# Kernel tuning notes

Hardware: AMD Instinct MI355X
Metric: run time of the kernel (lower is better)

## Reference

```python
import jax, jax.numpy as jnp
import numpy as np

N_GT, N_NODES, N_SPECIES, N_EDGES, D, L = 512, 399, 200, 397, 64, 2


def setup_inputs() -> dict:
    rng = np.random.default_rng(0)
    # Random recursive trees: parent of node i is uniform in [0, i).
    par = (rng.random((N_GT, N_NODES - 1)) * np.arange(1, N_NODES)).astype(np.int64)
    child = np.broadcast_to(np.arange(1, N_NODES), (N_GT, N_NODES - 1))
    off = (np.arange(N_GT, dtype=np.int64) * N_NODES)[:, None]
    c = (child + off).ravel()
    p = (par + off).ravel()
    # Both directions, as in the original [2, 2E_gt] convention.
    edge_index = np.stack([np.concatenate([c, p]), np.concatenate([p, c])])
    sp = np.full(N_NODES, -1, dtype=np.int64)
    sp[:N_SPECIES] = np.arange(N_SPECIES)
    sp_ids = np.tile(sp, N_GT)
    leaf_mask = sp_ids >= 0
    batch_vec = np.repeat(np.arange(N_GT, dtype=np.int64), N_NODES)
    # Clades: random species subsets per species-tree edge, guaranteed nonempty.
    pe = rng.uniform(0.05, 0.5, (N_EDGES, 1))
    clade_mask = rng.random((N_EDGES, N_SPECIES)) < pe
    clade_mask[np.arange(N_EDGES), rng.integers(0, N_SPECIES, N_EDGES)] = True
    key = jax.random.key(0)
    ks = jax.random.split(key, 3)
    s = 1.0 / np.sqrt(D)
    return {
        "edge_index": jnp.asarray(edge_index),
        "sp_ids": jnp.asarray(sp_ids),
        "leaf_mask": jnp.asarray(leaf_mask),
        "batch_vec": jnp.asarray(batch_vec),
        "clade_mask": jnp.asarray(clade_mask),
        "n_gt": N_GT,
        "emb_table": jax.random.normal(ks[0], (N_SPECIES + 1, D), jnp.float32),
        "W1": jax.random.normal(ks[1], (L, D, D), jnp.float32) * s,
        "b1": jnp.zeros((L, D), jnp.float32),
        "W2": jax.random.normal(ks[2], (L, D, D), jnp.float32) * s,
        "b2": jnp.zeros((L, D), jnp.float32),
        "eps": jnp.zeros((L,), jnp.float32),  # GINConv train_eps init 0
        "ln_gamma": jnp.ones((L, D), jnp.float32),
        "ln_beta": jnp.zeros((L, D), jnp.float32),
    }


def _layernorm(x, g, b):
    mu = x.mean(-1, keepdims=True)
    var = ((x - mu) ** 2).mean(-1, keepdims=True)
    return (x - mu) * jax.lax.rsqrt(var + 1e-5) * g + b


def reference(edge_index, sp_ids, leaf_mask, batch_vec, clade_mask, n_gt,
              emb_table, W1, b1, W2, b2, eps, ln_gamma, ln_beta):
    n_nodes = sp_ids.shape[0]
    n_edges, n_species = clade_mask.shape
    d = emb_table.shape[1]
    # Species embedding (internal nodes -> extra row n_species).
    emb_ids = jnp.where(sp_ids < 0, n_species, sp_ids)
    x = emb_table[emb_ids]  # [Nn, D]
    src, dst = edge_index[0], edge_index[1]
    for l in range(W1.shape[0]):
        # GINConv: mlp((1+eps)*x + sum_neighbors x_j), residual, LayerNorm.
        msg = jax.ops.segment_sum(x[src], dst, num_segments=n_nodes)
        h = (1.0 + eps[l]) * x + msg
        h = jax.nn.relu(h @ W1[l] + b1[l]) @ W2[l] + b2[l]
        x = _layernorm(x + h, ln_gamma[l], ln_beta[l])
        # dropout is identity in eval mode
    # Species pooling: mean over valid leaves per (gene tree, species).
    w = (leaf_mask & (sp_ids >= 0)).astype(x.dtype)  # [Nn]
    comp = batch_vec * n_species + jnp.maximum(sp_ids, 0)
    pool_size = n_gt * n_species
    sums = jax.ops.segment_sum(x * w[:, None], comp, num_segments=pool_size)
    cnts = jax.ops.segment_sum(w, comp, num_segments=pool_size)
    pool = (sums / jnp.maximum(cnts, 1.0)[:, None]).reshape(n_gt, n_species, d)
    valid = (cnts > 0).astype(x.dtype).reshape(n_gt, n_species)  # [G, S]
    # Clade pooling per species-tree edge (vectorized over the per-edge loop).
    mf = clade_mask.astype(x.dtype)  # [E, S]
    csum = jnp.einsum('es,gsd->egd', mf, pool * valid[:, :, None])  # [E,G,D]
    ccnt = mf @ valid.T  # [E, G] valid-species count per (edge, gene tree)
    gt_means = csum / jnp.maximum(ccnt, 1.0)[:, :, None]
    has = (ccnt > 0).astype(x.dtype)  # gene trees with data for this edge
    n_v = has.sum(1)  # [E]
    mean = (gt_means * has[:, :, None]).sum(1) / jnp.maximum(n_v, 1.0)[:, None]
    diff = (gt_means - mean[:, None, :]) * has[:, :, None]
    var = (diff ** 2).sum(1) / jnp.maximum(n_v - 1.0, 1.0)[:, None]  # unbiased
    ok = (n_v > 1)[:, None]
    std = jnp.where(ok, jnp.sqrt(jnp.where(ok, var, 1.0)), 0.0)
    mean = jnp.where((n_v > 0)[:, None], mean, 0.0)
    return jnp.concatenate([mean, std], axis=-1)  # [n_edges, 2*D]
```

## Files before the change

### kernel.cpp

```cpp
#include <hip/hip_runtime.h>

#define SMAX 200
#define NPG 399

typedef __bf16 bf16x8 __attribute__((ext_vector_type(8)));
typedef _Float16 half8 __attribute__((ext_vector_type(8)));
typedef float f32x4 __attribute__((ext_vector_type(4)));

__device__ __forceinline__ unsigned short f2bf(float f) {
  unsigned u = __float_as_uint(f);
  unsigned r = (u + 0x7FFFu + ((u >> 16) & 1u)) >> 16;
  return (unsigned short)r;
}
__device__ __forceinline__ int xel(int node, int dim) {
  return node * 64 + ((((dim >> 3)) ^ (node & 7)) << 3) + (dim & 7);
}

__global__ __launch_bounds__(256) void k_prep(const int* __restrict__ clade,
                                              unsigned short* __restrict__ mfA,
                                              unsigned* __restrict__ mfbits,
                                              int n_edges, int n_species) {
  int stride = gridDim.x * 256;
  for (int idx = blockIdx.x * 256 + threadIdx.x; idx < 25 * 7 * 512;
       idx += stride) {
    int fi = idx >> 9, within = idx & 511;
    int mt = fi / 7, kt = fi % 7;
    int l = within >> 3, j = within & 7;
    int e = mt * 16 + (l & 15);
    int s = kt * 32 + ((l >> 4) & 3) * 8 + j;
    unsigned short v = 0;
    if (e < n_edges && s < n_species && clade[(size_t)e * n_species + s] != 0)
      v = 0x3F80;
    mfA[idx] = v;
  }
  for (int idx = blockIdx.x * 256 + threadIdx.x; idx < 400 * 8; idx += stride) {
    int e = idx >> 3, w = idx & 7;
    unsigned bits = 0;
    if (e < n_edges && w < 7) {
      for (int b = 0; b < 32; ++b) {
        int s = w * 32 + b;
        if (s < n_species && clade[(size_t)e * n_species + s] != 0)
          bits |= 1u << b;
      }
    }
    mfbits[idx] = bits;
  }
}

__global__ __launch_bounds__(512) void k_tree(
    const float* __restrict__ emb, const int* __restrict__ sp,
    const int* __restrict__ leaf, const int* __restrict__ src,
    const int* __restrict__ dst, const float* __restrict__ W1,
    const float* __restrict__ b1, const float* __restrict__ W2,
    const float* __restrict__ b2, const float* __restrict__ eps_p,
    const float* __restrict__ gam, const float* __restrict__ bet,
    const unsigned short* __restrict__ mfA, const unsigned* __restrict__ mfbits,
    _Float16* __restrict__ gmat, float* __restrict__ has, int npg,
    int n_species, int n_edges, int n_gt) {
  __shared__ __attribute__((aligned(16))) _Float16 sA[NPG * 64];
  __shared__ __attribute__((aligned(16))) _Float16 sB[NPG * 64];
  __shared__ __attribute__((aligned(16))) _Float16 sWf[2][2][4096];
  __shared__ __attribute__((aligned(16))) _Float16 sT[8][1024];
  __shared__ int sStart[NPG + 1];
  __shared__ int sChild[NPG - 1];
  __shared__ int sPar[NPG];
  __shared__ int sCnt[NPG];

  int g = blockIdx.x, tid = threadIdx.x;
  int base = g * npg, nEt = npg - 1, ebase = g * nEt;
  int w = tid >> 6, lane = tid & 63;
  int cc = lane & 15, gq = lane >> 4;

  for (int i = tid; i < npg + 1; i += 512) sStart[i] = 0;
  for (int i = tid; i < npg; i += 512) sCnt[i] = 0;
  __syncthreads();
  for (int idx = tid; idx < 4096; idx += 512) {
    int k = idx >> 6, n = idx & 63;
    int frag = (k >> 5) * 4 + (n >> 4);
    int ln = ((k >> 3) & 3) * 16 + (n & 15);
    int j = k & 7;
    int o = frag * 512 + ln * 8 + j;
    sWf[0][0][o] = (_Float16)W1[idx];
    sWf[0][1][o] = (_Float16)W2[idx];
    sWf[1][0][o] = (_Float16)W1[4096 + idx];
    sWf[1][1][o] = (_Float16)W2[4096 + idx];
  }
  for (int idx = tid; idx < npg * 8; idx += 512) {
    int node = idx >> 3, ch = idx & 7;
    int s = sp[base + node];
    int row = (s < 0) ? n_species : s;
    float4 v0 = reinterpret_cast<const float4*>(emb)[row * 16 + ch * 2];
    float4 v1 = reinterpret_cast<const float4*>(emb)[row * 16 + ch * 2 + 1];
    half8 h;
    h[0] = (_Float16)v0.x; h[1] = (_Float16)v0.y;
    h[2] = (_Float16)v0.z; h[3] = (_Float16)v0.w;
    h[4] = (_Float16)v1.x; h[5] = (_Float16)v1.y;
    h[6] = (_Float16)v1.z; h[7] = (_Float16)v1.w;
    *reinterpret_cast<half8*>(&sA[node * 64 + ((ch ^ (node & 7)) << 3)]) = h;
  }
  for (int i = tid; i < nEt; i += 512) {
    int c = src[ebase + i] - base;
    int p = dst[ebase + i] - base;
    sPar[c] = p;
    atomicAdd(&sStart[p + 1], 1);
  }
  __syncthreads();
  if (w == 0) {
    int run = 0;
    for (int chunk = 0; chunk * 64 < npg + 1; ++chunk) {
      int idx = chunk * 64 + lane;
      int v = (idx < npg + 1) ? sStart[idx] : 0;
      for (int off = 1; off < 64; off <<= 1) {
        int t2 = __shfl_up(v, off);
        if (lane >= off) v += t2;
      }
      v += run;
      if (idx < npg + 1) sStart[idx] = v;
      run = __shfl(v, 63);
    }
  }
  __syncthreads();
  for (int c = tid + 1; c < npg; c += 512) {
    int p = sPar[c];
    int pos = sStart[p] + atomicAdd(&sCnt[p], 1);
    sChild[pos] = c;
  }
  __syncthreads();

  _Float16* tb = sT[w];
  int t0w = w * 3;
  int t1w = (w == 7) ? 25 : t0w + 3;
  for (int l = 0; l < 2; ++l) {
    const _Float16* xin = l ? sB : sA;
    _Float16* xout = l ? sA : sB;
    const half8* xin8 = reinterpret_cast<const half8*>(xin);
    float e1 = 1.0f + eps_p[l];
    float b1v[4], b2v[4], gv[4], bv[4];
#pragma unroll
    for (int nt = 0; nt < 4; ++nt) {
      b1v[nt] = b1[l * 64 + cc + 16 * nt];
      b2v[nt] = b2[l * 64 + cc + 16 * nt];
      gv[nt] = gam[l * 64 + cc + 16 * nt];
      bv[nt] = bet[l * 64 + cc + 16 * nt];
    }
    const half8* B1 = reinterpret_cast<const half8*>(sWf[l][0]);
    const half8* B2 = reinterpret_cast<const half8*>(sWf[l][1]);
    for (int t = t0w; t < t1w; ++t) {
      int n0 = t * 16;
      int node = n0 + cc;
      bool vn = node < npg;
      int nd2 = vn ? node : 0;
      int j0v = vn ? sStart[nd2] : 0;
      int cnt = vn ? (sStart[nd2 + 1] - j0v) : 0;
      half8 s0 = xin8[nd2 * 8 + (gq ^ (nd2 & 7))];
      half8 s1 = xin8[nd2 * 8 + ((4 + gq) ^ (nd2 & 7))];
      bool hasp = vn && node > 0;
      int pr = hasp ? sPar[nd2] : 0;
      half8 p0 = xin8[pr * 8 + (gq ^ (pr & 7))];
      half8 p1 = xin8[pr * 8 + ((4 + gq) ^ (pr & 7))];
      float a0f[8], a1f[8];
#pragma unroll
      for (int d = 0; d < 8; ++d) {
        a0f[d] = e1 * (float)s0[d] + (hasp ? (float)p0[d] : 0.f);
        a1f[d] = e1 * (float)s1[d] + (hasp ? (float)p1[d] : 0.f);
      }
      int cmax = cnt;
#pragma unroll
      for (int off = 1; off < 64; off <<= 1)
        cmax = max(cmax, __shfl_xor(cmax, off));
      cmax = __builtin_amdgcn_readfirstlane(cmax);
      for (int k0 = 0; k0 < cmax; k0 += 4) {
        int ci[4];
#pragma unroll
        for (int jj = 0; jj < 4; ++jj) {
          int kk = k0 + jj;
          ci[jj] = sChild[(kk < cnt) ? (j0v + kk) : 0];
        }
        half8 v0[4], v1[4];
#pragma unroll
        for (int jj = 0; jj < 4; ++jj) {
          int c = ci[jj];
          v0[jj] = xin8[c * 8 + (gq ^ (c & 7))];
          v1[jj] = xin8[c * 8 + ((4 + gq) ^ (c & 7))];
        }
#pragma unroll
        for (int jj = 0; jj < 4; ++jj) {
          if (k0 + jj < cnt) {
#pragma unroll
            for (int d = 0; d < 8; ++d) {
              a0f[d] += (float)v0[jj][d];
              a1f[d] += (float)v1[jj][d];
            }
          }
        }
      }
      half8 a0, a1;
#pragma unroll
      for (int d = 0; d < 8; ++d) {
        a0[d] = (_Float16)a0f[d];
        a1[d] = (_Float16)a1f[d];
      }
      f32x4 tacc[4];
#pragma unroll
      for (int nt = 0; nt < 4; ++nt) tacc[nt] = (f32x4){0.f, 0.f, 0.f, 0.f};
#pragma unroll
      for (int nt = 0; nt < 4; ++nt) {
        tacc[nt] = __builtin_amdgcn_mfma_f32_16x16x32_f16(
            a0, B1[nt * 64 + lane], tacc[nt], 0, 0, 0);
        tacc[nt] = __builtin_amdgcn_mfma_f32_16x16x32_f16(
            a1, B1[(4 + nt) * 64 + lane], tacc[nt], 0, 0, 0);
      }
#pragma unroll
      for (int nt = 0; nt < 4; ++nt)
#pragma unroll
        for (int r = 0; r < 4; ++r) {
          int m = gq * 4 + r;
          tb[m * 64 + ((cc + 16 * nt) ^ ((m & 7) << 3))] =
              (_Float16)fmaxf(tacc[nt][r] + b1v[nt], 0.f);
        }
      int sw = (cc & 7) << 3;
      half8 c0 =
          *reinterpret_cast<const half8*>(&tb[cc * 64 + ((gq * 8) ^ sw)]);
      half8 c1 =
          *reinterpret_cast<const half8*>(&tb[cc * 64 + ((32 + gq * 8) ^ sw)]);
      f32x4 hacc[4];
#pragma unroll
      for (int nt = 0; nt < 4; ++nt) hacc[nt] = (f32x4){0.f, 0.f, 0.f, 0.f};
#pragma unroll
      for (int nt = 0; nt < 4; ++nt) {
        hacc[nt] = __builtin_amdgcn_mfma_f32_16x16x32_f16(
            c0, B2[nt * 64 + lane], hacc[nt], 0, 0, 0);
        hacc[nt] = __builtin_amdgcn_mfma_f32_16x16x32_f16(
            c1, B2[(4 + nt) * 64 + lane], hacc[nt], 0, 0, 0);
      }
      float y[4][4];
#pragma unroll
      for (int r = 0; r < 4; ++r) {
        int nd3 = n0 + gq * 4 + r;
        bool v3 = nd3 < npg;
        int nds = v3 ? nd3 : 0;
#pragma unroll
        for (int nt = 0; nt < 4; ++nt) {
          float xv = (float)xin[xel(nds, cc + 16 * nt)];
          y[r][nt] = (v3 ? xv : 0.f) + hacc[nt][r] + b2v[nt];
        }
      }
#pragma unroll
      for (int r = 0; r < 4; ++r) {
        float s = y[r][0] + y[r][1] + y[r][2] + y[r][3];
        s += __shfl_xor(s, 1);
        s += __shfl_xor(s, 2);
        s += __shfl_xor(s, 4);
        s += __shfl_xor(s, 8);
        float mu = s * (1.f / 64.f);
        float d0 = y[r][0] - mu, d1 = y[r][1] - mu;
        float d2 = y[r][2] - mu, d3 = y[r][3] - mu;
        float v = d0 * d0 + d1 * d1 + d2 * d2 + d3 * d3;
        v += __shfl_xor(v, 1);
        v += __shfl_xor(v, 2);
        v += __shfl_xor(v, 4);
        v += __shfl_xor(v, 8);
        float iv = rsqrtf(v * (1.f / 64.f) + 1e-5f);
        int nd3 = n0 + gq * 4 + r;
        if (nd3 < npg) {
#pragma unroll
          for (int nt = 0; nt < 4; ++nt)
            xout[xel(nd3, cc + 16 * nt)] =
                (_Float16)((y[r][nt] - mu) * iv * gv[nt] + bv[nt]);
        }
      }
    }
    __syncthreads();
  }

  unsigned short* sBfU = reinterpret_cast<unsigned short*>(&sWf[0][0][0]);
  char* aux = reinterpret_cast<char*>(&sT[0][0]);
  float* sInv = reinterpret_cast<float*>(aux);
  float* sHas = reinterpret_cast<float*>(aux + 1600);
  unsigned* svb = reinterpret_cast<unsigned*>(aux + 3200);
  for (int i = tid; i < n_species + 1; i += 512) sStart[i] = 0;
  for (int i = tid; i < n_species; i += 512) sCnt[i] = 0;
  {
    float4 z4 = {0.f, 0.f, 0.f, 0.f};
    for (int i = tid; i < 1792; i += 512)
      reinterpret_cast<float4*>(sBfU)[i] = z4;
  }
  __syncthreads();
  for (int i = tid; i < npg; i += 512) {
    int s = sp[base + i];
    if (s >= 0 && leaf[base + i] != 0) atomicAdd(&sStart[s + 1], 1);
  }
  __syncthreads();
  if (w == 0) {
    int run = 0;
    for (int chunk = 0; chunk * 64 < n_species + 1; ++chunk) {
      int idx = chunk * 64 + lane;
      int v = (idx < n_species + 1) ? sStart[idx] : 0;
      for (int off = 1; off < 64; off <<= 1) {
        int t2 = __shfl_up(v, off);
        if (lane >= off) v += t2;
      }
      v += run;
      if (idx < n_species + 1) sStart[idx] = v;
      run = __shfl(v, 63);
    }
  }
  __syncthreads();
  for (int i = tid; i < npg; i += 512) {
    int s = sp[base + i];
    if (s >= 0 && leaf[base + i] != 0) {
      int pos = sStart[s] + atomicAdd(&sCnt[s], 1);
      sPar[pos] = i;
    }
  }
  __syncthreads();
  for (int idx = tid; idx < n_species * 8; idx += 512) {
    int s = idx >> 3, dc = idx & 7;
    int j0 = sStart[s], j1 = sStart[s + 1];
    float sum[8] = {0.f, 0.f, 0.f, 0.f, 0.f, 0.f, 0.f, 0.f};
    for (int j2 = j0; j2 < j1; ++j2) {
      int nd = sPar[j2];
      half8 v = *reinterpret_cast<const half8*>(
          &sA[nd * 64 + ((dc ^ (nd & 7)) << 3)]);
#pragma unroll
      for (int dd = 0; dd < 8; ++dd) sum[dd] += (float)v[dd];
    }
    float invc = (j1 > j0) ? 1.f / (float)(j1 - j0) : 0.f;
#pragma unroll
    for (int dd = 0; dd < 8; ++dd) {
      int d = dc * 8 + dd;
      int frag = (s >> 5) * 4 + (d >> 4);
      int ln = ((s >> 3) & 3) * 16 + (d & 15);
      sBfU[frag * 512 + ln * 8 + (s & 7)] = f2bf(sum[dd] * invc);
    }
  }
  if (tid < 7) {
    unsigned bits = 0;
    for (int b = 0; b < 32; ++b) {
      int s = tid * 32 + b;
      if (s < n_species && sStart[s + 1] > sStart[s]) bits |= 1u << b;
    }
    svb[tid] = bits;
  }
  __syncthreads();
  for (int e = tid; e < 400; e += 512) {
    unsigned ccv = 0;
#pragma unroll
    for (int w2 = 0; w2 < 7; ++w2) ccv += __popc(mfbits[e * 8 + w2] & svb[w2]);
    sInv[e] = 1.f / (float)max(ccv, 1u);
    sHas[e] = (ccv > 0) ? 1.f : 0.f;
  }
  __syncthreads();
  const bf16x8* A = reinterpret_cast<const bf16x8*>(mfA);
  const bf16x8* Bb = reinterpret_cast<const bf16x8*>(sBfU);
  for (int mt = w; mt < 25; mt += 8) {
    bf16x8 af[7];
#pragma unroll
    for (int kt = 0; kt < 7; ++kt) af[kt] = A[(mt * 7 + kt) * 64 + lane];
    f32x4 acc0 = {0.f, 0.f, 0.f, 0.f};
    f32x4 acc1 = {0.f, 0.f, 0.f, 0.f};
    f32x4 acc2 = {0.f, 0.f, 0.f, 0.f};
    f32x4 acc3 = {0.f, 0.f, 0.f, 0.f};
#pragma unroll
    for (int kt = 0; kt < 7; ++kt) {
      const bf16x8* B = Bb + kt * 256 + lane;
      acc0 = __builtin_amdgcn_mfma_f32_16x16x32_bf16(af[kt], B[0], acc0, 0, 0, 0);
      acc1 = __builtin_amdgcn_mfma_f32_16x16x32_bf16(af[kt], B[64], acc1, 0, 0, 0);
      acc2 = __builtin_amdgcn_mfma_f32_16x16x32_bf16(af[kt], B[128], acc2, 0, 0, 0);
      acc3 = __builtin_amdgcn_mfma_f32_16x16x32_bf16(af[kt], B[192], acc3, 0, 0, 0);
    }
    int rbase = mt * 16 + (lane >> 4) * 4;
    int col = lane & 15;
#pragma unroll
    for (int r = 0; r < 4; ++r) {
      int e = rbase + r;
      if (e >= n_edges) continue;
      float inv = sInv[e];
      _Float16* gp = gmat + ((size_t)e * n_gt + g) * 64 + col;
      gp[0] = (_Float16)(acc0[r] * inv);
      gp[16] = (_Float16)(acc1[r] * inv);
      gp[32] = (_Float16)(acc2[r] * inv);
      gp[48] = (_Float16)(acc3[r] * inv);
      if (col == 0) has[(size_t)e * n_gt + g] = sHas[e];
    }
  }
}

__global__ __launch_bounds__(256) void k_stat2(const _Float16* __restrict__ gmat,
                                               const float* __restrict__ has,
                                               float* __restrict__ part,
                                               int n_gt) {
  __shared__ float red1[4][64];
  __shared__ float red2[4][64];
  __shared__ float redn[4];
  int b = blockIdx.x;
  int e = b >> 2, q = b & 3;
  int tid = threadIdx.x, w = tid >> 6, lane = tid & 63;
  const _Float16* ge = gmat + ((size_t)e * n_gt + q * 128) * 64;
  const float* he = has + (size_t)e * n_gt + q * 128;
  float S1 = 0.f, S2 = 0.f, nv = 0.f;
  for (int i = w; i < 128; i += 4) {
    float h = he[i];
    float v = (float)ge[i * 64 + lane];
    S1 += h * v;
    S2 += h * v * v;
    nv += h;
  }
  red1[w][lane] = S1;
  red2[w][lane] = S2;
  if (lane == 0) redn[w] = nv;
  __syncthreads();
  if (w == 0) {
    float s1 = 0.f, s2 = 0.f, n_v = 0.f;
#pragma unroll
    for (int j = 0; j < 4; ++j) {
      s1 += red1[j][lane];
      s2 += red2[j][lane];
      n_v += redn[j];
    }
    float* p = part + (size_t)b * 130;
    p[lane] = s1;
    p[64 + lane] = s2;
    if (lane == 0) p[128] = n_v;
  }
}

__global__ __launch_bounds__(64) void k_fin(const float* __restrict__ part,
                                            float* __restrict__ out) {
  int e = blockIdx.x;
  int lane = threadIdx.x;
  float s1 = 0.f, s2 = 0.f, n_v = 0.f;
#pragma unroll
  for (int q = 0; q < 4; ++q) {
    const float* p = part + (size_t)(e * 4 + q) * 130;
    s1 += p[lane];
    s2 += p[64 + lane];
    n_v += p[128];
  }
  float mean = s1 / fmaxf(n_v, 1.f);
  float var = (s2 - s1 * s1 / fmaxf(n_v, 1.f)) / fmaxf(n_v - 1.f, 1.f);
  float stdv = (n_v > 1.f) ? sqrtf(fmaxf(var, 0.f)) : 0.f;
  out[(size_t)e * 128 + lane] = (n_v > 0.f) ? mean : 0.f;
  out[(size_t)e * 128 + 64 + lane] = stdv;
}

extern "C" void kernel_launch(void* const* d_in, const int* in_sizes, int n_in,
                              void* d_out, int out_size, void* d_ws, size_t ws_size,
                              hipStream_t stream) {
  (void)n_in; (void)out_size; (void)ws_size;
  const int* edge_index = (const int*)d_in[0];
  const int* sp_ids = (const int*)d_in[1];
  const int* leaf_mask = (const int*)d_in[2];
  const int* clade_mask = (const int*)d_in[4];
  const float* emb = (const float*)d_in[6];
  const float* W1 = (const float*)d_in[7];
  const float* b1 = (const float*)d_in[8];
  const float* W2 = (const float*)d_in[9];
  const float* b2 = (const float*)d_in[10];
  const float* eps = (const float*)d_in[11];
  const float* lng = (const float*)d_in[12];
  const float* lnb = (const float*)d_in[13];
  float* out = (float*)d_out;

  const int n_nodes = in_sizes[1];
  const int nE = in_sizes[0] / 2;
  const int n_species = in_sizes[6] / 64 - 1;
  const int n_edges = in_sizes[4] / n_species;
  const int n_gt = 512;
  const int npg = n_nodes / n_gt;

  const int* src = edge_index;
  const int* dst = edge_index + nE;

  _Float16* gmat = (_Float16*)d_ws;
  size_t gsz =
      ((size_t)n_edges * n_gt * 64 * sizeof(_Float16) + 255ul) & ~255ul;
  float* has = (float*)((char*)d_ws + gsz);
  size_t hsz = ((size_t)n_edges * n_gt * sizeof(float) + 255ul) & ~255ul;
  unsigned short* mfA = (unsigned short*)((char*)d_ws + gsz + hsz);
  size_t masz = ((size_t)25 * 7 * 512 * sizeof(unsigned short) + 255ul) & ~255ul;
  unsigned* mfbits = (unsigned*)((char*)d_ws + gsz + hsz + masz);
  size_t mbsz = ((size_t)400 * 8 * sizeof(unsigned) + 255ul) & ~255ul;
  float* part = (float*)((char*)d_ws + gsz + hsz + masz + mbsz);

  k_prep<<<64, 256, 0, stream>>>(clade_mask, mfA, mfbits, n_edges, n_species);
  k_tree<<<n_gt, 512, 0, stream>>>(emb, sp_ids, leaf_mask, src, dst, W1, b1,
                                   W2, b2, eps, lng, lnb, mfA, mfbits, gmat,
                                   has, npg, n_species, n_edges, n_gt);
  k_stat2<<<n_edges * 4, 256, 0, stream>>>(gmat, has, part, n_gt);
  k_fin<<<n_edges, 64, 0, stream>>>(part, out);
}
```

Before: 116.9 us.

## Double k_tree block size and update node features in place

Launches the per-gene-tree kernel with 1024 threads (16 waves) instead of 512. Each wave now handles at most two 16-node tiles per GIN layer instead of three. The second LDS feature buffer is removed: each wave gathers its aggregated inputs and residual values into registers, then a barrier separates the reads from the in-place writes back to sA. This cuts LDS use and raises per-block parallelism. In exchange it adds a block-wide barrier per layer and more register pressure under the 1024-thread launch bound.

```diff
diff --git a/kernel.cpp b/kernel.cpp
--- a/kernel.cpp
+++ b/kernel.cpp
@@ -47,7 +47,7 @@
   }
 }
 
-__global__ __launch_bounds__(512) void k_tree(
+__global__ __launch_bounds__(1024) void k_tree(
     const float* __restrict__ emb, const int* __restrict__ sp,
     const int* __restrict__ leaf, const int* __restrict__ src,
     const int* __restrict__ dst, const float* __restrict__ W1,
@@ -58,9 +58,8 @@
     _Float16* __restrict__ gmat, float* __restrict__ has, int npg,
     int n_species, int n_edges, int n_gt) {
   __shared__ __attribute__((aligned(16))) _Float16 sA[NPG * 64];
-  __shared__ __attribute__((aligned(16))) _Float16 sB[NPG * 64];
   __shared__ __attribute__((aligned(16))) _Float16 sWf[2][2][4096];
-  __shared__ __attribute__((aligned(16))) _Float16 sT[8][1024];
+  __shared__ __attribute__((aligned(16))) _Float16 sT[16][1024];
   __shared__ int sStart[NPG + 1];
   __shared__ int sChild[NPG - 1];
   __shared__ int sPar[NPG];
@@ -71,10 +70,10 @@
   int w = tid >> 6, lane = tid & 63;
   int cc = lane & 15, gq = lane >> 4;
 
-  for (int i = tid; i < npg + 1; i += 512) sStart[i] = 0;
-  for (int i = tid; i < npg; i += 512) sCnt[i] = 0;
-  __syncthreads();
-  for (int idx = tid; idx < 4096; idx += 512) {
+  for (int i = tid; i < npg + 1; i += 1024) sStart[i] = 0;
+  for (int i = tid; i < npg; i += 1024) sCnt[i] = 0;
+  __syncthreads();
+  for (int idx = tid; idx < 4096; idx += 1024) {
     int k = idx >> 6, n = idx & 63;
     int frag = (k >> 5) * 4 + (n >> 4);
     int ln = ((k >> 3) & 3) * 16 + (n & 15);
@@ -85,7 +84,7 @@
     sWf[1][0][o] = (_Float16)W1[4096 + idx];
     sWf[1][1][o] = (_Float16)W2[4096 + idx];
   }
-  for (int idx = tid; idx < npg * 8; idx += 512) {
+  for (int idx = tid; idx < npg * 8; idx += 1024) {
     int node = idx >> 3, ch = idx & 7;
     int s = sp[base + node];
     int row = (s < 0) ? n_species : s;
@@ -98,7 +97,7 @@
     h[6] = (_Float16)v1.z; h[7] = (_Float16)v1.w;
     *reinterpret_cast<half8*>(&sA[node * 64 + ((ch ^ (node & 7)) << 3)]) = h;
   }
-  for (int i = tid; i < nEt; i += 512) {
+  for (int i = tid; i < nEt; i += 1024) {
     int c = src[ebase + i] - base;
     int p = dst[ebase + i] - base;
     sPar[c] = p;
@@ -120,7 +119,7 @@
     }
   }
   __syncthreads();
-  for (int c = tid + 1; c < npg; c += 512) {
+  for (int c = tid + 1; c < npg; c += 1024) {
     int p = sPar[c];
     int pos = sStart[p] + atomicAdd(&sCnt[p], 1);
     sChild[pos] = c;
@@ -128,12 +127,9 @@
   __syncthreads();
 
   _Float16* tb = sT[w];
-  int t0w = w * 3;
-  int t1w = (w == 7) ? 25 : t0w + 3;
+  const _Float16* xin = sA;
+  const half8* xin8 = reinterpret_cast<const half8*>(sA);
   for (int l = 0; l < 2; ++l) {
-    const _Float16* xin = l ? sB : sA;
-    _Float16* xout = l ? sA : sB;
-    const half8* xin8 = reinterpret_cast<const half8*>(xin);
     float e1 = 1.0f + eps_p[l];
     float b1v[4], b2v[4], gv[4], bv[4];
 #pragma unroll
@@ -145,10 +141,14 @@
     }
     const half8* B1 = reinterpret_cast<const half8*>(sWf[l][0]);
     const half8* B2 = reinterpret_cast<const half8*>(sWf[l][1]);
-    for (int t = t0w; t < t1w; ++t) {
+    half8 aT0[2], aT1[2], rA[2], rB[2];
+#pragma unroll
+    for (int ti = 0; ti < 2; ++ti) {
+      int t = ti ? (16 + w) : w;
+      bool tv = t < 25;
       int n0 = t * 16;
       int node = n0 + cc;
-      bool vn = node < npg;
+      bool vn = tv && node < npg;
       int nd2 = vn ? node : 0;
       int j0v = vn ? sStart[nd2] : 0;
       int cnt = vn ? (sStart[nd2 + 1] - j0v) : 0;
@@ -194,21 +194,38 @@
           }
         }
       }
-      half8 a0, a1;
 #pragma unroll
       for (int d = 0; d < 8; ++d) {
-        a0[d] = (_Float16)a0f[d];
-        a1[d] = (_Float16)a1f[d];
-      }
+        aT0[ti][d] = (_Float16)a0f[d];
+        aT1[ti][d] = (_Float16)a1f[d];
+      }
+#pragma unroll
+      for (int r = 0; r < 4; ++r)
+#pragma unroll
+        for (int nt = 0; nt < 4; ++nt) {
+          int nd3 = n0 + gq * 4 + r;
+          _Float16 v = (tv && nd3 < npg) ? xin[xel(nd3, cc + 16 * nt)]
+                                         : (_Float16)0.f;
+          int idx = r * 4 + nt;
+          if (idx < 8) rA[ti][idx] = v;
+          else rB[ti][idx - 8] = v;
+        }
+    }
+    __syncthreads();
+#pragma unroll
+    for (int ti = 0; ti < 2; ++ti) {
+      int t = ti ? (16 + w) : w;
+      if (t >= 25) continue;
+      int n0 = t * 16;
       f32x4 tacc[4];
 #pragma unroll
       for (int nt = 0; nt < 4; ++nt) tacc[nt] = (f32x4){0.f, 0.f, 0.f, 0.f};
 #pragma unroll
       for (int nt = 0; nt < 4; ++nt) {
         tacc[nt] = __builtin_amdgcn_mfma_f32_16x16x32_f16(
-            a0, B1[nt * 64 + lane], tacc[nt], 0, 0, 0);
+            aT0[ti], B1[nt * 64 + lane], tacc[nt], 0, 0, 0);
         tacc[nt] = __builtin_amdgcn_mfma_f32_16x16x32_f16(
-            a1, B1[(4 + nt) * 64 + lane], tacc[nt], 0, 0, 0);
+            aT1[ti], B1[(4 + nt) * 64 + lane], tacc[nt], 0, 0, 0);
       }
 #pragma unroll
       for (int nt = 0; nt < 4; ++nt)
@@ -235,16 +252,13 @@
       }
       float y[4][4];
 #pragma unroll
-      for (int r = 0; r < 4; ++r) {
-        int nd3 = n0 + gq * 4 + r;
-        bool v3 = nd3 < npg;
-        int nds = v3 ? nd3 : 0;
+      for (int r = 0; r < 4; ++r)
 #pragma unroll
         for (int nt = 0; nt < 4; ++nt) {
-          float xv = (float)xin[xel(nds, cc + 16 * nt)];
-          y[r][nt] = (v3 ? xv : 0.f) + hacc[nt][r] + b2v[nt];
-        }
-      }
+          int idx = r * 4 + nt;
+          float xv = (idx < 8) ? (float)rA[ti][idx] : (float)rB[ti][idx - 8];
+          y[r][nt] = xv + hacc[nt][r] + b2v[nt];
+        }
 #pragma unroll
       for (int r = 0; r < 4; ++r) {
         float s = y[r][0] + y[r][1] + y[r][2] + y[r][3];
@@ -265,7 +279,7 @@
         if (nd3 < npg) {
 #pragma unroll
           for (int nt = 0; nt < 4; ++nt)
-            xout[xel(nd3, cc + 16 * nt)] =
+            sA[xel(nd3, cc + 16 * nt)] =
                 (_Float16)((y[r][nt] - mu) * iv * gv[nt] + bv[nt]);
         }
       }
@@ -278,15 +292,15 @@
   float* sInv = reinterpret_cast<float*>(aux);
   float* sHas = reinterpret_cast<float*>(aux + 1600);
   unsigned* svb = reinterpret_cast<unsigned*>(aux + 3200);
-  for (int i = tid; i < n_species + 1; i += 512) sStart[i] = 0;
-  for (int i = tid; i < n_species; i += 512) sCnt[i] = 0;
+  for (int i = tid; i < n_species + 1; i += 1024) sStart[i] = 0;
+  for (int i = tid; i < n_species; i += 1024) sCnt[i] = 0;
   {
     float4 z4 = {0.f, 0.f, 0.f, 0.f};
-    for (int i = tid; i < 1792; i += 512)
+    for (int i = tid; i < 1792; i += 1024)
       reinterpret_cast<float4*>(sBfU)[i] = z4;
   }
   __syncthreads();
-  for (int i = tid; i < npg; i += 512) {
+  for (int i = tid; i < npg; i += 1024) {
     int s = sp[base + i];
     if (s >= 0 && leaf[base + i] != 0) atomicAdd(&sStart[s + 1], 1);
   }
@@ -306,7 +320,7 @@
     }
   }
   __syncthreads();
-  for (int i = tid; i < npg; i += 512) {
+  for (int i = tid; i < npg; i += 1024) {
     int s = sp[base + i];
     if (s >= 0 && leaf[base + i] != 0) {
       int pos = sStart[s] + atomicAdd(&sCnt[s], 1);
@@ -314,7 +328,7 @@
     }
   }
   __syncthreads();
-  for (int idx = tid; idx < n_species * 8; idx += 512) {
+  for (int idx = tid; idx < n_species * 8; idx += 1024) {
     int s = idx >> 3, dc = idx & 7;
     int j0 = sStart[s], j1 = sStart[s + 1];
     float sum[8] = {0.f, 0.f, 0.f, 0.f, 0.f, 0.f, 0.f, 0.f};
@@ -343,7 +357,7 @@
     svb[tid] = bits;
   }
   __syncthreads();
-  for (int e = tid; e < 400; e += 512) {
+  for (int e = tid; e < 400; e += 1024) {
     unsigned ccv = 0;
 #pragma unroll
     for (int w2 = 0; w2 < 7; ++w2) ccv += __popc(mfbits[e * 8 + w2] & svb[w2]);
@@ -353,7 +367,7 @@
   __syncthreads();
   const bf16x8* A = reinterpret_cast<const bf16x8*>(mfA);
   const bf16x8* Bb = reinterpret_cast<const bf16x8*>(sBfU);
-  for (int mt = w; mt < 25; mt += 8) {
+  for (int mt = w; mt < 25; mt += 16) {
     bf16x8 af[7];
 #pragma unroll
     for (int kt = 0; kt < 7; ++kt) af[kt] = A[(mt * 7 + kt) * 64 + lane];
@@ -484,9 +498,9 @@
   float* part = (float*)((char*)d_ws + gsz + hsz + masz + mbsz);
 
   k_prep<<<64, 256, 0, stream>>>(clade_mask, mfA, mfbits, n_edges, n_species);
-  k_tree<<<n_gt, 512, 0, stream>>>(emb, sp_ids, leaf_mask, src, dst, W1, b1,
-                                   W2, b2, eps, lng, lnb, mfA, mfbits, gmat,
-                                   has, npg, n_species, n_edges, n_gt);
+  k_tree<<<n_gt, 1024, 0, stream>>>(emb, sp_ids, leaf_mask, src, dst, W1, b1,
+                                    W2, b2, eps, lng, lnb, mfA, mfbits, gmat,
+                                    has, npg, n_species, n_edges, n_gt);
   k_stat2<<<n_edges * 4, 256, 0, stream>>>(gmat, has, part, n_gt);
   k_fin<<<n_edges, 64, 0, stream>>>(part, out);
 }
```

Measured after the change: 226.7 us. 93.9% more time.

## Split tree kernel, move weight swizzle to prep, cut LDS for occupancy

Applied to the files above, without the earlier changes.

The weight fp16 swizzle moves into the prep kernel, so each tree block reads MFMA B fragments from global memory (cached) and no longer holds 32KB of shared weights. The clade-pooling GEMM is split into a new kernel that reads per-tree pooled bf16 tiles and valid bits staged in global memory. This lowers LDS use in k_tree and sets launch bounds to 4 blocks per CU for higher occupancy. The child aggregation loop is also simplified to one child per iteration. The cost is an extra launch, a global round trip for the pooled data, and weight fragments fetched from global memory rather than LDS.

```diff
diff --git a/kernel.cpp b/kernel.cpp
--- a/kernel.cpp
+++ b/kernel.cpp
@@ -1,6 +1,5 @@
 #include <hip/hip_runtime.h>
 
-#define SMAX 200
 #define NPG 399
 
 typedef __bf16 bf16x8 __attribute__((ext_vector_type(8)));
@@ -17,8 +16,11 @@
 }
 
 __global__ __launch_bounds__(256) void k_prep(const int* __restrict__ clade,
+                                              const float* __restrict__ W1,
+                                              const float* __restrict__ W2,
                                               unsigned short* __restrict__ mfA,
                                               unsigned* __restrict__ mfbits,
+                                              _Float16* __restrict__ wswz,
                                               int n_edges, int n_species) {
   int stride = gridDim.x * 256;
   for (int idx = blockIdx.x * 256 + threadIdx.x; idx < 25 * 7 * 512;
@@ -45,21 +47,28 @@
     }
     mfbits[idx] = bits;
   }
-}
-
-__global__ __launch_bounds__(512) void k_tree(
+  for (int idx = blockIdx.x * 256 + threadIdx.x; idx < 16384; idx += stride) {
+    int li = idx >> 12;
+    int k = (idx >> 6) & 63, n = idx & 63;
+    int frag = (k >> 5) * 4 + (n >> 4);
+    int ln = ((k >> 3) & 3) * 16 + (n & 15);
+    int j = k & 7;
+    int l = li >> 1;
+    const float* Ws = (li & 1) ? W2 : W1;
+    wswz[li * 4096 + frag * 512 + ln * 8 + j] = (_Float16)Ws[l * 4096 + k * 64 + n];
+  }
+}
+
+__global__ __launch_bounds__(512, 4) void k_tree(
     const float* __restrict__ emb, const int* __restrict__ sp,
     const int* __restrict__ leaf, const int* __restrict__ src,
-    const int* __restrict__ dst, const float* __restrict__ W1,
-    const float* __restrict__ b1, const float* __restrict__ W2,
-    const float* __restrict__ b2, const float* __restrict__ eps_p,
-    const float* __restrict__ gam, const float* __restrict__ bet,
-    const unsigned short* __restrict__ mfA, const unsigned* __restrict__ mfbits,
-    _Float16* __restrict__ gmat, float* __restrict__ has, int npg,
-    int n_species, int n_edges, int n_gt) {
+    const int* __restrict__ dst, const _Float16* __restrict__ wswz,
+    const float* __restrict__ b1, const float* __restrict__ b2,
+    const float* __restrict__ eps_p, const float* __restrict__ gam,
+    const float* __restrict__ bet, unsigned short* __restrict__ pool_swz,
+    unsigned* __restrict__ valid_bits, int npg, int n_species) {
   __shared__ __attribute__((aligned(16))) _Float16 sA[NPG * 64];
   __shared__ __attribute__((aligned(16))) _Float16 sB[NPG * 64];
-  __shared__ __attribute__((aligned(16))) _Float16 sWf[2][2][4096];
   __shared__ __attribute__((aligned(16))) _Float16 sT[8][1024];
   __shared__ int sStart[NPG + 1];
   __shared__ int sChild[NPG - 1];
@@ -74,17 +83,6 @@
   for (int i = tid; i < npg + 1; i += 512) sStart[i] = 0;
   for (int i = tid; i < npg; i += 512) sCnt[i] = 0;
   __syncthreads();
-  for (int idx = tid; idx < 4096; idx += 512) {
-    int k = idx >> 6, n = idx & 63;
-    int frag = (k >> 5) * 4 + (n >> 4);
-    int ln = ((k >> 3) & 3) * 16 + (n & 15);
-    int j = k & 7;
-    int o = frag * 512 + ln * 8 + j;
-    sWf[0][0][o] = (_Float16)W1[idx];
-    sWf[0][1][o] = (_Float16)W2[idx];
-    sWf[1][0][o] = (_Float16)W1[4096 + idx];
-    sWf[1][1][o] = (_Float16)W2[4096 + idx];
-  }
   for (int idx = tid; idx < npg * 8; idx += 512) {
     int node = idx >> 3, ch = idx & 7;
     int s = sp[base + node];
@@ -143,8 +141,8 @@
       gv[nt] = gam[l * 64 + cc + 16 * nt];
       bv[nt] = bet[l * 64 + cc + 16 * nt];
     }
-    const half8* B1 = reinterpret_cast<const half8*>(sWf[l][0]);
-    const half8* B2 = reinterpret_cast<const half8*>(sWf[l][1]);
+    const half8* B1 = reinterpret_cast<const half8*>(wswz + (l * 2 + 0) * 4096);
+    const half8* B2 = reinterpret_cast<const half8*>(wswz + (l * 2 + 1) * 4096);
     for (int t = t0w; t < t1w; ++t) {
       int n0 = t * 16;
       int node = n0 + cc;
@@ -169,28 +167,18 @@
       for (int off = 1; off < 64; off <<= 1)
         cmax = max(cmax, __shfl_xor(cmax, off));
       cmax = __builtin_amdgcn_readfirstlane(cmax);
-      for (int k0 = 0; k0 < cmax; k0 += 4) {
-        int ci[4];
-#pragma unroll
-        for (int jj = 0; jj < 4; ++jj) {
-          int kk = k0 + jj;
-          ci[jj] = sChild[(kk < cnt) ? (j0v + kk) : 0];
-        }
-        half8 v0[4], v1[4];
-#pragma unroll
-        for (int jj = 0; jj < 4; ++jj) {
-          int c = ci[jj];
-          v0[jj] = xin8[c * 8 + (gq ^ (c & 7))];
-          v1[jj] = xin8[c * 8 + ((4 + gq) ^ (c & 7))];
-        }
-#pragma unroll
-        for (int jj = 0; jj < 4; ++jj) {
-          if (k0 + jj < cnt) {
-#pragma unroll
-            for (int d = 0; d < 8; ++d) {
-              a0f[d] += (float)v0[jj][d];
-              a1f[d] += (float)v1[jj][d];
-            }
+#pragma unroll 2
+      for (int k = 0; k < cmax; ++k) {
+        bool act = k < cnt;
+        int jidx = act ? (j0v + k) : 0;
+        int c = sChild[jidx];
+        half8 v0 = xin8[c * 8 + (gq ^ (c & 7))];
+        half8 v1 = xin8[c * 8 + ((4 + gq) ^ (c & 7))];
+        if (act) {
+#pragma unroll
+          for (int d = 0; d < 8; ++d) {
+            a0f[d] += (float)v0[d];
+            a1f[d] += (float)v1[d];
           }
         }
       }
@@ -273,18 +261,8 @@
     __syncthreads();
   }
 
-  unsigned short* sBfU = reinterpret_cast<unsigned short*>(&sWf[0][0][0]);
-  char* aux = reinterpret_cast<char*>(&sT[0][0]);
-  float* sInv = reinterpret_cast<float*>(aux);
-  float* sHas = reinterpret_cast<float*>(aux + 1600);
-  unsigned* svb = reinterpret_cast<unsigned*>(aux + 3200);
   for (int i = tid; i < n_species + 1; i += 512) sStart[i] = 0;
   for (int i = tid; i < n_species; i += 512) sCnt[i] = 0;
-  {
-    float4 z4 = {0.f, 0.f, 0.f, 0.f};
-    for (int i = tid; i < 1792; i += 512)
-      reinterpret_cast<float4*>(sBfU)[i] = z4;
-  }
   __syncthreads();
   for (int i = tid; i < npg; i += 512) {
     int s = sp[base + i];
@@ -314,24 +292,29 @@
     }
   }
   __syncthreads();
-  for (int idx = tid; idx < n_species * 8; idx += 512) {
+  unsigned short* pg = pool_swz + (size_t)g * 14336;
+  for (int idx = tid; idx < 224 * 8; idx += 512) {
     int s = idx >> 3, dc = idx & 7;
-    int j0 = sStart[s], j1 = sStart[s + 1];
     float sum[8] = {0.f, 0.f, 0.f, 0.f, 0.f, 0.f, 0.f, 0.f};
-    for (int j2 = j0; j2 < j1; ++j2) {
-      int nd = sPar[j2];
-      half8 v = *reinterpret_cast<const half8*>(
-          &sA[nd * 64 + ((dc ^ (nd & 7)) << 3)]);
-#pragma unroll
-      for (int dd = 0; dd < 8; ++dd) sum[dd] += (float)v[dd];
-    }
-    float invc = (j1 > j0) ? 1.f / (float)(j1 - j0) : 0.f;
+    int cntv = 0;
+    if (s < n_species) {
+      int j0 = sStart[s], j1 = sStart[s + 1];
+      cntv = j1 - j0;
+      for (int j2 = j0; j2 < j1; ++j2) {
+        int nd = sPar[j2];
+        half8 v = *reinterpret_cast<const half8*>(
+            &sA[nd * 64 + ((dc ^ (nd & 7)) << 3)]);
+#pragma unroll
+        for (int dd = 0; dd < 8; ++dd) sum[dd] += (float)v[dd];
+      }
+    }
+    float invc = (cntv > 0) ? 1.f / (float)cntv : 0.f;
 #pragma unroll
     for (int dd = 0; dd < 8; ++dd) {
       int d = dc * 8 + dd;
       int frag = (s >> 5) * 4 + (d >> 4);
       int ln = ((s >> 3) & 3) * 16 + (d & 15);
-      sBfU[frag * 512 + ln * 8 + (s & 7)] = f2bf(sum[dd] * invc);
+      pg[frag * 512 + ln * 8 + (s & 7)] = f2bf(sum[dd] * invc);
     }
   }
   if (tid < 7) {
@@ -340,19 +323,39 @@
       int s = tid * 32 + b;
       if (s < n_species && sStart[s + 1] > sStart[s]) bits |= 1u << b;
     }
-    svb[tid] = bits;
-  }
-  __syncthreads();
+    valid_bits[(size_t)g * 8 + tid] = bits;
+  }
+}
+
+__global__ __launch_bounds__(512) void k_gm2(
+    const unsigned short* __restrict__ pool_swz,
+    const unsigned* __restrict__ valid_bits,
+    const unsigned short* __restrict__ mfA, const unsigned* __restrict__ mfbits,
+    _Float16* __restrict__ gmat, float* __restrict__ has, int n_edges,
+    int n_gt) {
+  __shared__ __attribute__((aligned(16))) unsigned short sBf[14336];
+  __shared__ float sInv[400];
+  __shared__ float sHas[400];
+  int g = blockIdx.x;
+  int tid = threadIdx.x;
+  const float4* src4 =
+      reinterpret_cast<const float4*>(pool_swz + (size_t)g * 14336);
+  float4* dst4 = reinterpret_cast<float4*>(sBf);
+  for (int i = tid; i < 1792; i += 512) dst4[i] = src4[i];
+  unsigned vb[7];
+#pragma unroll
+  for (int w2 = 0; w2 < 7; ++w2) vb[w2] = valid_bits[(size_t)g * 8 + w2];
   for (int e = tid; e < 400; e += 512) {
-    unsigned ccv = 0;
-#pragma unroll
-    for (int w2 = 0; w2 < 7; ++w2) ccv += __popc(mfbits[e * 8 + w2] & svb[w2]);
-    sInv[e] = 1.f / (float)max(ccv, 1u);
-    sHas[e] = (ccv > 0) ? 1.f : 0.f;
-  }
-  __syncthreads();
+    unsigned cc = 0;
+#pragma unroll
+    for (int w2 = 0; w2 < 7; ++w2) cc += __popc(mfbits[e * 8 + w2] & vb[w2]);
+    sInv[e] = 1.f / (float)max(cc, 1u);
+    sHas[e] = (cc > 0) ? 1.f : 0.f;
+  }
+  __syncthreads();
+  int w = tid >> 6, lane = tid & 63;
   const bf16x8* A = reinterpret_cast<const bf16x8*>(mfA);
-  const bf16x8* Bb = reinterpret_cast<const bf16x8*>(sBfU);
+  const bf16x8* Bb = reinterpret_cast<const bf16x8*>(sBf);
   for (int mt = w; mt < 25; mt += 8) {
     bf16x8 af[7];
 #pragma unroll
@@ -482,11 +485,23 @@
   unsigned* mfbits = (unsigned*)((char*)d_ws + gsz + hsz + masz);
   size_t mbsz = ((size_t)400 * 8 * sizeof(unsigned) + 255ul) & ~255ul;
   float* part = (float*)((char*)d_ws + gsz + hsz + masz + mbsz);
-
-  k_prep<<<64, 256, 0, stream>>>(clade_mask, mfA, mfbits, n_edges, n_species);
-  k_tree<<<n_gt, 512, 0, stream>>>(emb, sp_ids, leaf_mask, src, dst, W1, b1,
-                                   W2, b2, eps, lng, lnb, mfA, mfbits, gmat,
-                                   has, npg, n_species, n_edges, n_gt);
+  size_t psz = ((size_t)n_edges * 4 * 130 * sizeof(float) + 255ul) & ~255ul;
+  unsigned short* pool_swz =
+      (unsigned short*)((char*)d_ws + gsz + hsz + masz + mbsz + psz);
+  size_t poolsz = ((size_t)n_gt * 14336 * sizeof(unsigned short) + 255ul) & ~255ul;
+  unsigned* valid_bits =
+      (unsigned*)((char*)d_ws + gsz + hsz + masz + mbsz + psz + poolsz);
+  size_t vbsz = ((size_t)n_gt * 8 * sizeof(unsigned) + 255ul) & ~255ul;
+  _Float16* wswz = (_Float16*)((char*)d_ws + gsz + hsz + masz + mbsz + psz +
+                               poolsz + vbsz);
+
+  k_prep<<<64, 256, 0, stream>>>(clade_mask, W1, W2, mfA, mfbits, wswz,
+                                 n_edges, n_species);
+  k_tree<<<n_gt, 512, 0, stream>>>(emb, sp_ids, leaf_mask, src, dst, wswz, b1,
+                                   b2, eps, lng, lnb, pool_swz, valid_bits,
+                                   npg, n_species);
+  k_gm2<<<n_gt, 512, 0, stream>>>(pool_swz, valid_bits, mfA, mfbits, gmat,
+                                  has, n_edges, n_gt);
   k_stat2<<<n_edges * 4, 256, 0, stream>>>(gmat, has, part, n_gt);
   k_fin<<<n_edges, 64, 0, stream>>>(part, out);
 }
```

New measurement: 123.8 us. +5.9%, slower.
